# Optimization experiments

Measured on AMD Instinct MI355X. Metric: run time of the kernel, lower is better.

The kernel has to match this reference:

```python
import jax, jax.numpy as jnp
import numpy as np

N = 100000
E = 1600000
D_IN = 128
D_OUT = 128
BN_EPS = 1e-5


def setup_inputs() -> dict:
    key = jax.random.key(0)
    k_x, k_src, k_dst, k_val, k_w = jax.random.split(key, 5)
    x = jax.random.normal(k_x, (N, D_IN), dtype=jnp.float32)
    edge_src = jax.random.randint(k_src, (E,), 0, N, dtype=jnp.int64)
    edge_dst = jax.random.randint(k_dst, (E,), 0, N, dtype=jnp.int64)
    edge_vals = jax.random.uniform(k_val, (E,), dtype=jnp.float32)
    # kaiming-uniform-like init for weight
    bound = float(np.sqrt(6.0 / D_IN))
    weight = jax.random.uniform(k_w, (D_IN, D_OUT), dtype=jnp.float32,
                                minval=-bound, maxval=bound)
    bias = jnp.zeros((D_OUT,), dtype=jnp.float32)
    gamma = jnp.ones((D_OUT,), dtype=jnp.float32)   # BatchNorm weight
    beta = jnp.zeros((D_OUT,), dtype=jnp.float32)   # BatchNorm bias
    return {"x": x, "edge_src": edge_src, "edge_dst": edge_dst,
            "edge_vals": edge_vals, "weight": weight, "bias": bias,
            "gamma": gamma, "beta": beta}


def reference(x, edge_src, edge_dst, edge_vals, weight, bias, gamma, beta):
    # SpMM: out[dst] += val * x[src]  (adj @ x with adj in COO form)
    msgs = x[edge_src] * edge_vals[:, None]            # [E, D_IN]
    agg = jax.ops.segment_sum(msgs, edge_dst, num_segments=N)  # [N, D_IN]
    # Dense linear
    h = jnp.dot(agg, weight) + bias                     # [N, D_OUT]
    # BatchNorm1d (training mode: batch statistics, biased variance)
    mean = jnp.mean(h, axis=0)
    var = jnp.mean(jnp.square(h - mean), axis=0)
    h_norm = (h - mean) * jax.lax.rsqrt(var + BN_EPS)
    return h_norm * gamma + beta
```

## Files before the change

### kernel.cpp

```cpp
#include <hip/hip_runtime.h>
#include <math.h>

#define D 128
#define BSHIFT 9
#define BROWS 512
#define TILE 8192
constexpr float BN_EPS = 1e-5f;
typedef unsigned long long ull;
typedef __attribute__((ext_vector_type(8))) short short8v;
typedef __attribute__((ext_vector_type(4))) float f32x4;

__device__ __forceinline__ unsigned f2bf_rne(float f) {
    unsigned u = __float_as_uint(f);
    return (u + 0x7FFFu + ((u >> 16) & 1u)) >> 16;
}
__device__ __forceinline__ float bf_lo(unsigned u) { return __uint_as_float(u << 16); }
__device__ __forceinline__ float bf_hi(unsigned u) { return __uint_as_float(u & 0xFFFF0000u); }
__device__ __forceinline__ void split_bf16(float f, unsigned& hi, unsigned& lo) {
    hi = f2bf_rne(f);
    lo = f2bf_rne(f - bf_lo(hi));
}

__global__ __launch_bounds__(256) void wprep_kernel(
    const float* __restrict__ W,
    unsigned short* __restrict__ whiT,
    unsigned short* __restrict__ wloT)
{
    int idx = blockIdx.x * 256 + threadIdx.x;
    if (idx < 128 * 128) {
        int k = idx >> 7, nn = idx & 127;
        unsigned hi, lo;
        split_bf16(W[idx], hi, lo);
        whiT[nn * 128 + k] = (unsigned short)hi;
        wloT[nn * 128 + k] = (unsigned short)lo;
    }
}

__global__ __launch_bounds__(256) void phase1_kernel(
    const float* __restrict__ A,
    const unsigned short* __restrict__ whiT,
    const unsigned short* __restrict__ wloT,
    unsigned* __restrict__ yb,
    int n,
    const int* __restrict__ esrc, const int* __restrict__ edst,
    const float* __restrict__ evals,
    uint2* __restrict__ slices,
    int* __restrict__ ofs_t,
    int B, int nwgA, int E)
{
    __shared__ __align__(16) char smem[34816];
    const int tid = threadIdx.x;

    if ((int)blockIdx.x < nwgA) {
        int* h   = (int*)smem;
        int* ps  = h + 256;
        int* cur = ps + 256;
        const int wg = blockIdx.x;
        const int e0 = wg * TILE;
        const int e1 = min(e0 + TILE, E);

        h[tid] = 0;
        __syncthreads();
        for (int e = e0 + tid; e < e1; e += 256)
            atomicAdd(&h[edst[e] >> BSHIFT], 1);
        __syncthreads();

        const int v = h[tid];
        ps[tid] = v;
        __syncthreads();
        for (int off = 1; off < 256; off <<= 1) {
            int t = (tid >= off) ? ps[tid - off] : 0;
            __syncthreads();
            if (tid >= off) ps[tid] += t;
            __syncthreads();
        }
        const int excl = ps[tid] - v;
        if (tid < B) {
            cur[tid] = excl;
            ofs_t[(size_t)tid * nwgA + wg] = excl;
        }
        if (tid == 0) ofs_t[(size_t)B * nwgA + wg] = e1 - e0;
        __syncthreads();

        uint2* slice = slices + (size_t)wg * TILE;
        for (int e = e0 + tid; e < e1; e += 256) {
            int d = edst[e];
            int b = d >> BSHIFT;
            int p = atomicAdd(&cur[b], 1);
            uint2 rec;
            rec.x = (unsigned)(d & (BROWS - 1)) | ((unsigned)esrc[e] << BSHIFT);
            rec.y = __float_as_uint(evals[e]);
            slice[p] = rec;
        }
    } else {
        unsigned short* xh = (unsigned short*)smem;
        unsigned short* xl = xh + 64 * 136;

        const int row0 = ((int)blockIdx.x - nwgA) * 64;
        const float4* A4 = (const float4*)(A + (size_t)row0 * D);

#pragma unroll
        for (int i = 0; i < 8; i++) {
            const int idx = tid + 256 * i;
            const int row = idx >> 5, c4 = idx & 31;
            float4 v = (row0 + row < n) ? A4[idx]
                                        : make_float4(0.f, 0.f, 0.f, 0.f);
            unsigned h0, h1, h2, h3, l0, l1, l2, l3;
            split_bf16(v.x, h0, l0); split_bf16(v.y, h1, l1);
            split_bf16(v.z, h2, l2); split_bf16(v.w, h3, l3);
            unsigned short* ph = xh + (size_t)row * 136 + c4 * 4;
            unsigned short* pl = xl + (size_t)row * 136 + c4 * 4;
            *(uint2*)ph = make_uint2(h0 | (h1 << 16), h2 | (h3 << 16));
            *(uint2*)pl = make_uint2(l0 | (l1 << 16), l2 | (l3 << 16));
        }
        __syncthreads();

        const int wv = tid >> 6;
        const int l  = tid & 63;
        const int lr = l & 15;
        const int lg = l >> 4;
        const int colbase = wv * 32;

        f32x4 acc[4][2];
#pragma unroll
        for (int rt = 0; rt < 4; rt++)
#pragma unroll
            for (int ct = 0; ct < 2; ct++)
                acc[rt][ct] = (f32x4){0.f, 0.f, 0.f, 0.f};

        for (int k0 = 0; k0 < 128; k0 += 32) {
            const int kf = k0 + lg * 8;
            short8v ah[4], al[4];
#pragma unroll
            for (int rt = 0; rt < 4; rt++) {
                const unsigned short* p = xh + (size_t)(16 * rt + lr) * 136 + kf;
                const unsigned short* q = xl + (size_t)(16 * rt + lr) * 136 + kf;
                ah[rt] = *(const short8v*)p;
                al[rt] = *(const short8v*)q;
            }
            short8v bh[2], bl[2];
#pragma unroll
            for (int ct = 0; ct < 2; ct++) {
                const int nidx = colbase + 16 * ct + lr;
                bh[ct] = *(const short8v*)(whiT + (size_t)nidx * 128 + kf);
                bl[ct] = *(const short8v*)(wloT + (size_t)nidx * 128 + kf);
            }
#pragma unroll
            for (int rt = 0; rt < 4; rt++)
#pragma unroll
                for (int ct = 0; ct < 2; ct++) {
                    acc[rt][ct] = __builtin_amdgcn_mfma_f32_16x16x32_bf16(
                        ah[rt], bh[ct], acc[rt][ct], 0, 0, 0);
                    acc[rt][ct] = __builtin_amdgcn_mfma_f32_16x16x32_bf16(
                        ah[rt], bl[ct], acc[rt][ct], 0, 0, 0);
                    acc[rt][ct] = __builtin_amdgcn_mfma_f32_16x16x32_bf16(
                        al[rt], bh[ct], acc[rt][ct], 0, 0, 0);
                }
        }
        __syncthreads();

        float* Cl = (float*)smem;
#pragma unroll
        for (int rt = 0; rt < 4; rt++)
#pragma unroll
            for (int ct = 0; ct < 2; ct++)
#pragma unroll
                for (int r = 0; r < 4; r++) {
                    const int row = 16 * rt + lg * 4 + r;
                    const int col = colbase + 16 * ct + lr;
                    Cl[row * 132 + col] = acc[rt][ct][r];
                }
        __syncthreads();

#pragma unroll
        for (int i = 0; i < 8; i++) {
            const int idx = tid + 256 * i;
            const int row = idx >> 5, p = idx & 31;
            const float* c4 = Cl + row * 132 + p * 4;
            uint2 o;
            o.x = f2bf_rne(c4[0]) | (f2bf_rne(c4[1]) << 16);
            o.y = f2bf_rne(c4[2]) | (f2bf_rne(c4[3]) << 16);
            if (row0 + row < n)
                ((uint2*)(yb + (size_t)(row0 + row) * 64))[p] = o;
        }
    }
}

__global__ __launch_bounds__(1024) void binB_kernel(
    const uint2* __restrict__ slices,
    const int* __restrict__ ofs_t,
    int* __restrict__ rowptr,
    ull* __restrict__ csr,
    int B, int nwgA, int n)
{
    __shared__ int srow[256];
    __shared__ int erow[256];
    __shared__ int red[256];
    __shared__ int hist[BROWS];
    __shared__ int curs[BROWS];
    __shared__ int ps[BROWS];
    __shared__ int s_bbase;

    const int tid  = threadIdx.x;
    const int b    = blockIdx.x;
    const int w    = tid >> 6;
    const int lane = tid & 63;

    for (int i = tid; i < nwgA; i += 1024) {
        srow[i] = ofs_t[(size_t)b * nwgA + i];
        erow[i] = ofs_t[(size_t)(b + 1) * nwgA + i];
    }
    if (tid < BROWS) hist[tid] = 0;
    __syncthreads();

    if (tid < 256) red[tid] = (tid < nwgA) ? srow[tid] : 0;
    __syncthreads();
    for (int off = 128; off > 0; off >>= 1) {
        if (tid < off) red[tid] += red[tid + off];
        __syncthreads();
    }
    if (tid == 0) s_bbase = red[0];
    __syncthreads();

    for (int wg = w; wg < nwgA; wg += 16) {
        const int s = srow[wg];
        const int e = erow[wg];
        const uint2* run = slices + (size_t)wg * TILE;
        for (int i = s + lane; i < e; i += 64)
            atomicAdd(&hist[run[i].x & (BROWS - 1)], 1);
    }
    __syncthreads();

    int v0 = 0;
    if (tid < BROWS) { v0 = hist[tid]; ps[tid] = v0; }
    __syncthreads();
    for (int off = 1; off < BROWS; off <<= 1) {
        int t = 0;
        if (tid < BROWS && tid >= off) t = ps[tid - off];
        __syncthreads();
        if (tid < BROWS) ps[tid] += t;
        __syncthreads();
    }
    if (tid < BROWS) {
        const int excl = s_bbase + ps[tid] - v0;
        curs[tid] = excl;
        const int r = (b << BSHIFT) + tid;
        if (r < n) rowptr[r] = excl + v0;
    }
    __syncthreads();

    for (int wg = w; wg < nwgA; wg += 16) {
        const int s = srow[wg];
        const int e = erow[wg];
        const uint2* run = slices + (size_t)wg * TILE;
        for (int i = s + lane; i < e; i += 64) {
            uint2 r = run[i];
            int pos = atomicAdd(&curs[r.x & (BROWS - 1)], 1);
            csr[pos] = ((ull)r.y << 32) | (r.x >> BSHIFT);
        }
    }
}

__global__ __launch_bounds__(256) void spmm_stats_kernel(
    const unsigned* __restrict__ yb,
    const int* __restrict__ rowptr,
    const ull* __restrict__ csr,
    float* __restrict__ h,
    float* __restrict__ stats,
    int n)
{
    __shared__ int   rp[65];
    __shared__ float ssum[128];
    __shared__ float ssq[128];

    const int tid       = threadIdx.x;
    const int blockRow0 = blockIdx.x * 64;
    const int wv        = tid >> 6;
    const int lane      = tid & 63;
    const int half      = lane >> 5;
    const int li        = lane & 31;
    const int rbase     = blockRow0 + wv * 16;

    if (tid < 128) { ssum[tid] = 0.f; ssq[tid] = 0.f; }
    if (tid < 65) {
        int idx = blockRow0 + tid - 1;
        rp[tid] = (idx < 0) ? 0 : rowptr[min(idx, n - 1)];
    }
    __syncthreads();

    float s0 = 0.f, s1 = 0.f, s2 = 0.f, s3 = 0.f;
    float q0 = 0.f, q1 = 0.f, q2 = 0.f, q3 = 0.f;

    if (rbase < n) {
        for (int pr = 0; pr < 16; pr += 2) {
            const int  rA    = rbase + pr + half;
            const bool rowOK = rA < n;
            const int  s_    = rowOK ? rp[rA - blockRow0]     : 0;
            const int  e_    = rowOK ? rp[rA - blockRow0 + 1] : 0;
            const int  nA    = e_ - s_;
            const int  nMax  = max(nA, __shfl_xor(nA, 32));

            float a0 = 0.f, a1 = 0.f, a2 = 0.f, a3 = 0.f;
            for (int i = 0; i < nMax; i += 8) {
                ull cd[8];
#pragma unroll
                for (int j = 0; j < 8; j++) {
                    int idx = s_ + i + j;
                    int ce  = (idx < e_) ? idx : (nA ? e_ - 1 : 0);
                    cd[j] = csr[ce];
                }
                uint2 u[8];
                float v[8];
#pragma unroll
                for (int j = 0; j < 8; j++) {
                    u[j] = *(const uint2*)(yb + (size_t)(unsigned)cd[j] * 64 + 2 * li);
                    v[j] = (s_ + i + j < e_)
                               ? __uint_as_float((unsigned)(cd[j] >> 32))
                               : 0.f;
                }
#pragma unroll
                for (int j = 0; j < 8; j++) {
                    a0 += v[j] * bf_lo(u[j].x);
                    a1 += v[j] * bf_hi(u[j].x);
                    a2 += v[j] * bf_lo(u[j].y);
                    a3 += v[j] * bf_hi(u[j].y);
                }
            }

            if (rowOK) {
                *(float4*)&h[(size_t)rA * D + 4 * li] = make_float4(a0, a1, a2, a3);
                s0 += a0; s1 += a1; s2 += a2; s3 += a3;
                q0 += a0 * a0; q1 += a1 * a1; q2 += a2 * a2; q3 += a3 * a3;
            }
        }

        atomicAdd(&ssum[4 * li + 0], s0); atomicAdd(&ssum[4 * li + 1], s1);
        atomicAdd(&ssum[4 * li + 2], s2); atomicAdd(&ssum[4 * li + 3], s3);
        atomicAdd(&ssq [4 * li + 0], q0); atomicAdd(&ssq [4 * li + 1], q1);
        atomicAdd(&ssq [4 * li + 2], q2); atomicAdd(&ssq [4 * li + 3], q3);
    }
    __syncthreads();
    if (tid < 128) {
        atomicAdd(&stats[tid],       ssum[tid]);
        atomicAdd(&stats[128 + tid], ssq[tid]);
    }
}

__global__ __launch_bounds__(256) void bn_apply_kernel(
    float* __restrict__ h,
    const float* __restrict__ stats,
    const float* __restrict__ gamma,
    const float* __restrict__ beta,
    int n)
{
    __shared__ float s_scale[128];
    __shared__ float s_shift[128];
    const int tid = threadIdx.x;
    if (tid < 128) {
        const float invn = 1.0f / (float)n;
        const float mean = stats[tid] * invn;
        const float var  = stats[128 + tid] * invn - mean * mean;
        const float inv  = rsqrtf(var + BN_EPS);
        const float g    = gamma[tid] * inv;
        s_scale[tid] = g;
        s_shift[tid] = beta[tid] - mean * g;
    }
    __syncthreads();

    float4* h4 = (float4*)h;
    const size_t total = (size_t)n * D / 4;
    const size_t stride = (size_t)gridDim.x * blockDim.x;
    for (size_t i = (size_t)blockIdx.x * blockDim.x + tid; i < total; i += stride) {
        float4 v = h4[i];
        const int c = (int)((i * 4) & (D - 1));
        v.x = v.x * s_scale[c]     + s_shift[c];
        v.y = v.y * s_scale[c + 1] + s_shift[c + 1];
        v.z = v.z * s_scale[c + 2] + s_shift[c + 2];
        v.w = v.w * s_scale[c + 3] + s_shift[c + 3];
        h4[i] = v;
    }
}

__global__ __launch_bounds__(256) void spmm_atomic_kernel(
    const float* __restrict__ x,
    const int* __restrict__ esrc, const int* __restrict__ edst,
    const float* __restrict__ eval, float* __restrict__ agg, int E)
{
    int wave  = (blockIdx.x * blockDim.x + threadIdx.x) >> 6;
    int lane  = threadIdx.x & 63;
    int nwave = (gridDim.x * blockDim.x) >> 6;
    for (int e = wave; e < E; e += nwave) {
        int   s = esrc[e];
        int   d = edst[e];
        float v = eval[e];
        const float2 xv = ((const float2*)(x + (size_t)s * D))[lane];
        float* ar = agg + (size_t)d * D + lane * 2;
        atomicAdd(ar,     xv.x * v);
        atomicAdd(ar + 1, xv.y * v);
    }
}

__global__ __launch_bounds__(256) void gemm_stats_kernel(
    const float* __restrict__ A,
    const float* __restrict__ W,
    float* __restrict__ h,
    float* __restrict__ stats,
    int n)
{
    __shared__ float sW[128 * 128];
    __shared__ float sA[32][128];
    const int tid = threadIdx.x;
    const float4* W4  = (const float4*)W;
    float4*       sW4 = (float4*)sW;
#pragma unroll
    for (int i = 0; i < 16; i++) sW4[tid + 256 * i] = W4[tid + 256 * i];
    const int row0 = blockIdx.x * 32;
    const float4* A4  = (const float4*)(A + (size_t)row0 * D);
    float4*       sA4 = (float4*)&sA[0][0];
#pragma unroll
    for (int i = 0; i < 4; i++) {
        int idx = tid + 256 * i;
        sA4[idx] = ((size_t)row0 * D + (size_t)idx * 4 < (size_t)n * D)
                       ? A4[idx] : make_float4(0.f, 0.f, 0.f, 0.f);
    }
    __syncthreads();
    const int tx = tid & 31, ty = tid >> 5, c0 = tx * 4;
    float acc[4][4] = {};
    for (int k = 0; k < 128; k++) {
        const float4 w = *(const float4*)&sW[k * 128 + c0];
#pragma unroll
        for (int j = 0; j < 4; j++) {
            const float a = sA[ty + 8 * j][k];
            acc[j][0] += a * w.x; acc[j][1] += a * w.y;
            acc[j][2] += a * w.z; acc[j][3] += a * w.w;
        }
    }
#pragma unroll
    for (int j = 0; j < 4; j++) {
        const int row = row0 + ty + 8 * j;
        if (row < n)
            *(float4*)&h[(size_t)row * D + c0] =
                make_float4(acc[j][0], acc[j][1], acc[j][2], acc[j][3]);
    }
    __syncthreads();
    float* csum = &sA[0][0];
    float* csq  = csum + 128;
    if (tid < 128) { csum[tid] = 0.f; csq[tid] = 0.f; }
    __syncthreads();
#pragma unroll
    for (int c = 0; c < 4; c++) {
        float s = 0.f, q = 0.f;
#pragma unroll
        for (int j = 0; j < 4; j++) { s += acc[j][c]; q += acc[j][c] * acc[j][c]; }
        atomicAdd(&csum[c0 + c], s);
        atomicAdd(&csq[c0 + c], q);
    }
    __syncthreads();
    if (tid < 128) {
        atomicAdd(&stats[tid],       csum[tid]);
        atomicAdd(&stats[128 + tid], csq[tid]);
    }
}

extern "C" void kernel_launch(void* const* d_in, const int* in_sizes, int n_in,
                              void* d_out, int out_size, void* d_ws, size_t ws_size,
                              hipStream_t stream)
{
    const float* x     = (const float*)d_in[0];
    const int*   esrc  = (const int*)d_in[1];
    const int*   edst  = (const int*)d_in[2];
    const float* evals = (const float*)d_in[3];
    const float* W     = (const float*)d_in[4];
    const float* gamma = (const float*)d_in[6];
    const float* beta  = (const float*)d_in[7];
    float* out = (float*)d_out;

    const int n = in_sizes[0] / D;
    const int E = in_sizes[1];

    const int B     = (n + BROWS - 1) >> BSHIFT;
    const int nwgA  = (E + TILE - 1) / TILE;
    const int ngemm = (n + 63) / 64;

    unsigned*       yb     = (unsigned*)d_ws;
    float*          stats  = (float*)(yb + (size_t)n * 64);
    unsigned short* whiT   = (unsigned short*)(stats + 256);
    unsigned short* wloT   = whiT + 16384;
    int*            ofs_t  = (int*)(wloT + 16384);
    int*            rowptr = ofs_t + (size_t)(B + 1) * nwgA;
    size_t w_off = (size_t)n * 64 + 256 + 16384
                 + (size_t)(B + 1) * nwgA + n;
    w_off += (w_off & 1);
    uint2* slices = (uint2*)((unsigned*)d_ws + w_off);
    ull*   csr    = (ull*)(slices + (size_t)nwgA * TILE);
    const size_t need = (w_off + (size_t)nwgA * TILE * 2 + (size_t)E * 2) * 4;

    if (ws_size >= need && B <= 256 && nwgA <= 256) {
        hipMemsetAsync(stats, 0, 256 * 4, stream);
        wprep_kernel<<<64, 256, 0, stream>>>(W, whiT, wloT);
        phase1_kernel<<<nwgA + ngemm, 256, 0, stream>>>(
            x, whiT, wloT, yb, n, esrc, edst, evals, slices, ofs_t, B, nwgA, E);
        binB_kernel<<<B, 1024, 0, stream>>>(
            slices, ofs_t, rowptr, csr, B, nwgA, n);
        spmm_stats_kernel<<<(n + 63) / 64, 256, 0, stream>>>(
            yb, rowptr, csr, out, stats, n);
        bn_apply_kernel<<<2048, 256, 0, stream>>>(out, stats, gamma, beta, n);
    } else {
        float* agg = (float*)d_ws;
        float* st  = agg + (size_t)n * D;
        hipMemsetAsync(d_ws, 0, ((size_t)n * D + 256) * 4, stream);
        spmm_atomic_kernel<<<4096, 256, 0, stream>>>(x, esrc, edst, evals, agg, E);
        gemm_stats_kernel<<<(n + 31) / 32, 256, 0, stream>>>(agg, W, out, st, n);
        bn_apply_kernel<<<2048, 256, 0, stream>>>(out, st, gamma, beta, n);
    }
}
```

Measured before the change: 291.6 us.

## Regroup stages: fuse weight prep into binning A, co-schedule GEMM with binning B

The weight bf16 split moves into the edge-binning kernel as extra blocks. The GEMM blocks move out of phase 1 and into the second binning kernel, so the GEMM runs concurrently with the CSR scatter instead of with the first binning pass. This removes one kernel launch. The GEMM blocks become 1024 threads over 128 rows, with each wave computing a 64x16 tile and 69KB of LDS per block. That larger LDS footprint may lower occupancy, and a wave now reuses each weight fragment across fewer output columns.

```diff
diff --git a/kernel.cpp b/kernel.cpp
--- a/kernel.cpp
+++ b/kernel.cpp
@@ -21,87 +21,161 @@
     lo = f2bf_rne(f - bf_lo(hi));
 }
 
-__global__ __launch_bounds__(256) void wprep_kernel(
+__global__ __launch_bounds__(1024) void binAw_kernel(
+    const int* __restrict__ esrc, const int* __restrict__ edst,
+    const float* __restrict__ evals,
+    uint2* __restrict__ slices,
+    int* __restrict__ ofs_t,
     const float* __restrict__ W,
     unsigned short* __restrict__ whiT,
-    unsigned short* __restrict__ wloT)
-{
-    int idx = blockIdx.x * 256 + threadIdx.x;
-    if (idx < 128 * 128) {
-        int k = idx >> 7, nn = idx & 127;
-        unsigned hi, lo;
-        split_bf16(W[idx], hi, lo);
-        whiT[nn * 128 + k] = (unsigned short)hi;
-        wloT[nn * 128 + k] = (unsigned short)lo;
-    }
-}
-
-__global__ __launch_bounds__(256) void phase1_kernel(
+    unsigned short* __restrict__ wloT,
+    int B, int nwgA, int E)
+{
+    __shared__ int h[256];
+    __shared__ int ps[256];
+    __shared__ int cur[256];
+    const int tid = threadIdx.x;
+
+    if ((int)blockIdx.x >= nwgA) {
+        int idx = ((int)blockIdx.x - nwgA) * 1024 + tid;
+        if (idx < 128 * 128) {
+            int k = idx >> 7, nn = idx & 127;
+            unsigned hi, lo;
+            split_bf16(W[idx], hi, lo);
+            whiT[nn * 128 + k] = (unsigned short)hi;
+            wloT[nn * 128 + k] = (unsigned short)lo;
+        }
+        return;
+    }
+
+    const int wg = blockIdx.x;
+    const int e0 = wg * TILE;
+    const int e1 = min(e0 + TILE, E);
+
+    if (tid < 256) h[tid] = 0;
+    __syncthreads();
+    for (int e = e0 + tid; e < e1; e += 1024)
+        atomicAdd(&h[edst[e] >> BSHIFT], 1);
+    __syncthreads();
+
+    int v = 0;
+    if (tid < 256) { v = h[tid]; ps[tid] = v; }
+    __syncthreads();
+    for (int off = 1; off < 256; off <<= 1) {
+        int t = 0;
+        if (tid < 256 && tid >= off) t = ps[tid - off];
+        __syncthreads();
+        if (tid < 256 && tid >= off) ps[tid] += t;
+        __syncthreads();
+    }
+    if (tid < B) {
+        cur[tid] = ps[tid] - v;
+        ofs_t[(size_t)tid * nwgA + wg] = ps[tid] - v;
+    }
+    if (tid == 0) ofs_t[(size_t)B * nwgA + wg] = e1 - e0;
+    __syncthreads();
+
+    uint2* slice = slices + (size_t)wg * TILE;
+    for (int e = e0 + tid; e < e1; e += 1024) {
+        int d = edst[e];
+        int p = atomicAdd(&cur[d >> BSHIFT], 1);
+        uint2 rec;
+        rec.x = (unsigned)(d & (BROWS - 1)) | ((unsigned)esrc[e] << BSHIFT);
+        rec.y = __float_as_uint(evals[e]);
+        slice[p] = rec;
+    }
+}
+
+__global__ __launch_bounds__(1024) void phase2_kernel(
+    const uint2* __restrict__ slices,
+    const int* __restrict__ ofs_t,
+    int* __restrict__ rowptr,
+    ull* __restrict__ csr,
     const float* __restrict__ A,
     const unsigned short* __restrict__ whiT,
     const unsigned short* __restrict__ wloT,
     unsigned* __restrict__ yb,
-    int n,
-    const int* __restrict__ esrc, const int* __restrict__ edst,
-    const float* __restrict__ evals,
-    uint2* __restrict__ slices,
-    int* __restrict__ ofs_t,
-    int B, int nwgA, int E)
-{
-    __shared__ __align__(16) char smem[34816];
+    int B, int nwgA, int n)
+{
+    __shared__ __align__(16) char smem[69632];
     const int tid = threadIdx.x;
 
-    if ((int)blockIdx.x < nwgA) {
-        int* h   = (int*)smem;
-        int* ps  = h + 256;
-        int* cur = ps + 256;
-        const int wg = blockIdx.x;
-        const int e0 = wg * TILE;
-        const int e1 = min(e0 + TILE, E);
-
-        h[tid] = 0;
-        __syncthreads();
-        for (int e = e0 + tid; e < e1; e += 256)
-            atomicAdd(&h[edst[e] >> BSHIFT], 1);
-        __syncthreads();
-
-        const int v = h[tid];
-        ps[tid] = v;
-        __syncthreads();
-        for (int off = 1; off < 256; off <<= 1) {
-            int t = (tid >= off) ? ps[tid - off] : 0;
+    if ((int)blockIdx.x < B) {
+        int* srow = (int*)smem;
+        int* erow = srow + 256;
+        int* red  = erow + 256;
+        int* hist = red + 256;
+        int* curs = hist + BROWS;
+        int* ps   = curs + BROWS;
+        int* s_bbase = ps + BROWS;
+
+        const int b    = blockIdx.x;
+        const int w    = tid >> 6;
+        const int lane = tid & 63;
+
+        for (int i = tid; i < nwgA; i += 1024) {
+            srow[i] = ofs_t[(size_t)b * nwgA + i];
+            erow[i] = ofs_t[(size_t)(b + 1) * nwgA + i];
+        }
+        if (tid < BROWS) hist[tid] = 0;
+        __syncthreads();
+
+        if (tid < 256) red[tid] = (tid < nwgA) ? srow[tid] : 0;
+        __syncthreads();
+        for (int off = 128; off > 0; off >>= 1) {
+            if (tid < off) red[tid] += red[tid + off];
             __syncthreads();
-            if (tid >= off) ps[tid] += t;
+        }
+        if (tid == 0) *s_bbase = red[0];
+        __syncthreads();
+
+        for (int wg = w; wg < nwgA; wg += 16) {
+            const int s = srow[wg];
+            const int e = erow[wg];
+            const uint2* run = slices + (size_t)wg * TILE;
+            for (int i = s + lane; i < e; i += 64)
+                atomicAdd(&hist[run[i].x & (BROWS - 1)], 1);
+        }
+        __syncthreads();
+
+        int v0 = 0;
+        if (tid < BROWS) { v0 = hist[tid]; ps[tid] = v0; }
+        __syncthreads();
+        for (int off = 1; off < BROWS; off <<= 1) {
+            int t = 0;
+            if (tid < BROWS && tid >= off) t = ps[tid - off];
             __syncthreads();
-        }
-        const int excl = ps[tid] - v;
-        if (tid < B) {
-            cur[tid] = excl;
-            ofs_t[(size_t)tid * nwgA + wg] = excl;
-        }
-        if (tid == 0) ofs_t[(size_t)B * nwgA + wg] = e1 - e0;
-        __syncthreads();
-
-        uint2* slice = slices + (size_t)wg * TILE;
-        for (int e = e0 + tid; e < e1; e += 256) {
-            int d = edst[e];
-            int b = d >> BSHIFT;
-            int p = atomicAdd(&cur[b], 1);
-            uint2 rec;
-            rec.x = (unsigned)(d & (BROWS - 1)) | ((unsigned)esrc[e] << BSHIFT);
-            rec.y = __float_as_uint(evals[e]);
-            slice[p] = rec;
+            if (tid < BROWS) ps[tid] += t;
+            __syncthreads();
+        }
+        if (tid < BROWS) {
+            const int excl = *s_bbase + ps[tid] - v0;
+            curs[tid] = excl;
+            const int r = (b << BSHIFT) + tid;
+            if (r < n) rowptr[r] = excl + v0;
+        }
+        __syncthreads();
+
+        for (int wg = w; wg < nwgA; wg += 16) {
+            const int s = srow[wg];
+            const int e = erow[wg];
+            const uint2* run = slices + (size_t)wg * TILE;
+            for (int i = s + lane; i < e; i += 64) {
+                uint2 r = run[i];
+                int pos = atomicAdd(&curs[r.x & (BROWS - 1)], 1);
+                csr[pos] = ((ull)r.y << 32) | (r.x >> BSHIFT);
+            }
         }
     } else {
         unsigned short* xh = (unsigned short*)smem;
-        unsigned short* xl = xh + 64 * 136;
-
-        const int row0 = ((int)blockIdx.x - nwgA) * 64;
+        unsigned short* xl = xh + 128 * 136;
+
+        const int row0 = ((int)blockIdx.x - B) * 128;
         const float4* A4 = (const float4*)(A + (size_t)row0 * D);
 
 #pragma unroll
-        for (int i = 0; i < 8; i++) {
-            const int idx = tid + 256 * i;
+        for (int i = 0; i < 4; i++) {
+            const int idx = tid + 1024 * i;
             const int row = idx >> 5, c4 = idx & 31;
             float4 v = (row0 + row < n) ? A4[idx]
                                         : make_float4(0.f, 0.f, 0.f, 0.f);
@@ -119,43 +193,34 @@
         const int l  = tid & 63;
         const int lr = l & 15;
         const int lg = l >> 4;
-        const int colbase = wv * 32;
-
-        f32x4 acc[4][2];
+        const int rowbase = (wv >> 3) * 64;
+        const int colbase = (wv & 7) * 16;
+
+        f32x4 acc[4];
 #pragma unroll
         for (int rt = 0; rt < 4; rt++)
-#pragma unroll
-            for (int ct = 0; ct < 2; ct++)
-                acc[rt][ct] = (f32x4){0.f, 0.f, 0.f, 0.f};
+            acc[rt] = (f32x4){0.f, 0.f, 0.f, 0.f};
 
         for (int k0 = 0; k0 < 128; k0 += 32) {
             const int kf = k0 + lg * 8;
             short8v ah[4], al[4];
 #pragma unroll
             for (int rt = 0; rt < 4; rt++) {
-                const unsigned short* p = xh + (size_t)(16 * rt + lr) * 136 + kf;
-                const unsigned short* q = xl + (size_t)(16 * rt + lr) * 136 + kf;
+                const unsigned short* p =
+                    xh + (size_t)(rowbase + 16 * rt + lr) * 136 + kf;
+                const unsigned short* q =
+                    xl + (size_t)(rowbase + 16 * rt + lr) * 136 + kf;
                 ah[rt] = *(const short8v*)p;
                 al[rt] = *(const short8v*)q;
             }
-            short8v bh[2], bl[2];
-#pragma unroll
-            for (int ct = 0; ct < 2; ct++) {
-                const int nidx = colbase + 16 * ct + lr;
-                bh[ct] = *(const short8v*)(whiT + (size_t)nidx * 128 + kf);
-                bl[ct] = *(const short8v*)(wloT + (size_t)nidx * 128 + kf);
+            const short8v bh = *(const short8v*)(whiT + (size_t)(colbase + lr) * 128 + kf);
+            const short8v bl = *(const short8v*)(wloT + (size_t)(colbase + lr) * 128 + kf);
+#pragma unroll
+            for (int rt = 0; rt < 4; rt++) {
+                acc[rt] = __builtin_amdgcn_mfma_f32_16x16x32_bf16(ah[rt], bh, acc[rt], 0, 0, 0);
+                acc[rt] = __builtin_amdgcn_mfma_f32_16x16x32_bf16(ah[rt], bl, acc[rt], 0, 0, 0);
+                acc[rt] = __builtin_amdgcn_mfma_f32_16x16x32_bf16(al[rt], bh, acc[rt], 0, 0, 0);
             }
-#pragma unroll
-            for (int rt = 0; rt < 4; rt++)
-#pragma unroll
-                for (int ct = 0; ct < 2; ct++) {
-                    acc[rt][ct] = __builtin_amdgcn_mfma_f32_16x16x32_bf16(
-                        ah[rt], bh[ct], acc[rt][ct], 0, 0, 0);
-                    acc[rt][ct] = __builtin_amdgcn_mfma_f32_16x16x32_bf16(
-                        ah[rt], bl[ct], acc[rt][ct], 0, 0, 0);
-                    acc[rt][ct] = __builtin_amdgcn_mfma_f32_16x16x32_bf16(
-                        al[rt], bh[ct], acc[rt][ct], 0, 0, 0);
-                }
         }
         __syncthreads();
 
@@ -163,18 +228,15 @@
 #pragma unroll
         for (int rt = 0; rt < 4; rt++)
 #pragma unroll
-            for (int ct = 0; ct < 2; ct++)
-#pragma unroll
-                for (int r = 0; r < 4; r++) {
-                    const int row = 16 * rt + lg * 4 + r;
-                    const int col = colbase + 16 * ct + lr;
-                    Cl[row * 132 + col] = acc[rt][ct][r];
-                }
-        __syncthreads();
-
-#pragma unroll
-        for (int i = 0; i < 8; i++) {
-            const int idx = tid + 256 * i;
+            for (int r = 0; r < 4; r++) {
+                const int row = rowbase + 16 * rt + lg * 4 + r;
+                Cl[row * 132 + colbase + lr] = acc[rt][r];
+            }
+        __syncthreads();
+
+#pragma unroll
+        for (int i = 0; i < 4; i++) {
+            const int idx = tid + 1024 * i;
             const int row = idx >> 5, p = idx & 31;
             const float* c4 = Cl + row * 132 + p * 4;
             uint2 o;
@@ -182,81 +244,6 @@
             o.y = f2bf_rne(c4[2]) | (f2bf_rne(c4[3]) << 16);
             if (row0 + row < n)
                 ((uint2*)(yb + (size_t)(row0 + row) * 64))[p] = o;
-        }
-    }
-}
-
-__global__ __launch_bounds__(1024) void binB_kernel(
-    const uint2* __restrict__ slices,
-    const int* __restrict__ ofs_t,
-    int* __restrict__ rowptr,
-    ull* __restrict__ csr,
-    int B, int nwgA, int n)
-{
-    __shared__ int srow[256];
-    __shared__ int erow[256];
-    __shared__ int red[256];
-    __shared__ int hist[BROWS];
-    __shared__ int curs[BROWS];
-    __shared__ int ps[BROWS];
-    __shared__ int s_bbase;
-
-    const int tid  = threadIdx.x;
-    const int b    = blockIdx.x;
-    const int w    = tid >> 6;
-    const int lane = tid & 63;
-
-    for (int i = tid; i < nwgA; i += 1024) {
-        srow[i] = ofs_t[(size_t)b * nwgA + i];
-        erow[i] = ofs_t[(size_t)(b + 1) * nwgA + i];
-    }
-    if (tid < BROWS) hist[tid] = 0;
-    __syncthreads();
-
-    if (tid < 256) red[tid] = (tid < nwgA) ? srow[tid] : 0;
-    __syncthreads();
-    for (int off = 128; off > 0; off >>= 1) {
-        if (tid < off) red[tid] += red[tid + off];
-        __syncthreads();
-    }
-    if (tid == 0) s_bbase = red[0];
-    __syncthreads();
-
-    for (int wg = w; wg < nwgA; wg += 16) {
-        const int s = srow[wg];
-        const int e = erow[wg];
-        const uint2* run = slices + (size_t)wg * TILE;
-        for (int i = s + lane; i < e; i += 64)
-            atomicAdd(&hist[run[i].x & (BROWS - 1)], 1);
-    }
-    __syncthreads();
-
-    int v0 = 0;
-    if (tid < BROWS) { v0 = hist[tid]; ps[tid] = v0; }
-    __syncthreads();
-    for (int off = 1; off < BROWS; off <<= 1) {
-        int t = 0;
-        if (tid < BROWS && tid >= off) t = ps[tid - off];
-        __syncthreads();
-        if (tid < BROWS) ps[tid] += t;
-        __syncthreads();
-    }
-    if (tid < BROWS) {
-        const int excl = s_bbase + ps[tid] - v0;
-        curs[tid] = excl;
-        const int r = (b << BSHIFT) + tid;
-        if (r < n) rowptr[r] = excl + v0;
-    }
-    __syncthreads();
-
-    for (int wg = w; wg < nwgA; wg += 16) {
-        const int s = srow[wg];
-        const int e = erow[wg];
-        const uint2* run = slices + (size_t)wg * TILE;
-        for (int i = s + lane; i < e; i += 64) {
-            uint2 r = run[i];
-            int pos = atomicAdd(&curs[r.x & (BROWS - 1)], 1);
-            csr[pos] = ((ull)r.y << 32) | (r.x >> BSHIFT);
         }
     }
 }
@@ -478,9 +465,9 @@
     const int n = in_sizes[0] / D;
     const int E = in_sizes[1];
 
-    const int B     = (n + BROWS - 1) >> BSHIFT;
-    const int nwgA  = (E + TILE - 1) / TILE;
-    const int ngemm = (n + 63) / 64;
+    const int B      = (n + BROWS - 1) >> BSHIFT;
+    const int nwgA   = (E + TILE - 1) / TILE;
+    const int ngemm  = (n + 127) / 128;
 
     unsigned*       yb     = (unsigned*)d_ws;
     float*          stats  = (float*)(yb + (size_t)n * 64);
@@ -497,11 +484,10 @@
 
     if (ws_size >= need && B <= 256 && nwgA <= 256) {
         hipMemsetAsync(stats, 0, 256 * 4, stream);
-        wprep_kernel<<<64, 256, 0, stream>>>(W, whiT, wloT);
-        phase1_kernel<<<nwgA + ngemm, 256, 0, stream>>>(
-            x, whiT, wloT, yb, n, esrc, edst, evals, slices, ofs_t, B, nwgA, E);
-        binB_kernel<<<B, 1024, 0, stream>>>(
-            slices, ofs_t, rowptr, csr, B, nwgA, n);
+        binAw_kernel<<<nwgA + 16, 1024, 0, stream>>>(
+            esrc, edst, evals, slices, ofs_t, W, whiT, wloT, B, nwgA, E);
+        phase2_kernel<<<B + ngemm, 1024, 0, stream>>>(
+            slices, ofs_t, rowptr, csr, x, whiT, wloT, yb, B, nwgA, n);
         spmm_stats_kernel<<<(n + 63) / 64, 256, 0, stream>>>(
             yb, rowptr, csr, out, stats, n);
         bn_apply_kernel<<<2048, 256, 0, stream>>>(out, stats, gamma, beta, n);
```

Result: faster. 276.7 us (-5.1%).
